# Kernel tuning notes

Hardware: AMD Instinct MI355X
Metric: run time of the kernel (lower is better)

The kernel has to match this reference:

```python
import jax, jax.numpy as jnp
import numpy as np


def setup_inputs() -> dict:
    key = jax.random.key(0)
    k1, k2, k3, k4 = jax.random.split(key, 4)
    B, L1, L2, H, A = 64, 512, 512, 1024, 1024
    reps_lt = jax.random.normal(k1, (B, L1, H), dtype=jnp.float32)
    reps_rt = jax.random.normal(k2, (B, L2, H), dtype=jnp.float32)
    mask_lt = jnp.ones((B, L1), dtype=jnp.float32)
    mask_rt = jnp.ones((B, L2), dtype=jnp.float32)
    # Keras 'uniform' initializer ~ U(-0.05, 0.05); scale similarly
    attn_w1 = jax.random.uniform(k3, (H, A), dtype=jnp.float32, minval=-0.05, maxval=0.05)
    diagonal_W = jax.random.uniform(k4, (1, 1, A), dtype=jnp.float32, minval=-0.05, maxval=0.05)
    return {
        "reps_lt": reps_lt,
        "reps_rt": reps_rt,
        "mask_lt": mask_lt,
        "mask_rt": mask_rt,
        "attn_w1": attn_w1,
        "diagonal_W": diagonal_W,
    }


def reference(reps_lt, reps_rt, mask_lt, mask_rt, attn_w1, diagonal_W):
    # Projections: the original does expand_dims + broadcast multiply + sum,
    # which is mathematically a matmul over the hidden dim.
    # attn_w2 aliases attn_w1 because hidden dims are equal.
    attn_lt = jnp.tanh(jnp.einsum('blh,ha->bla', reps_lt, attn_w1))  # [B,L1,A]
    attn_rt = jnp.tanh(jnp.einsum('brh,ha->bra', reps_rt, attn_w1))  # [B,L2,A]
    attn_lt = attn_lt * diagonal_W                                   # diagonal bilinear scale
    # batch_dot([B,L1,A], [B,A,L2]) -> [B,L1,L2]
    attn_value = jnp.einsum('bla,bra->blr', attn_lt, attn_rt)
    # mask (multiplicative, as in original) before softmax
    attn_value = attn_value * mask_lt[:, :, None] * mask_rt[:, None, :]
    attn_prob = jax.nn.softmax(attn_value, axis=-1)
    # mask again after softmax
    attn_prob = attn_prob * mask_lt[:, :, None] * mask_rt[:, None, :]
    return attn_prob
```

## Files before the change

kernel.cpp:

```cpp
#include <hip/hip_runtime.h>
#include <hip/hip_bf16.h>

#define B_ 64
#define L_ 512
#define H_ 1024
#define A_ 1024

typedef short bf16x8 __attribute__((ext_vector_type(8)));
typedef float f32x4 __attribute__((ext_vector_type(4)));

__device__ __forceinline__ void gld16(const void* g, void* l) {
  __builtin_amdgcn_global_load_lds((const __attribute__((address_space(1))) void*)g,
                                   (__attribute__((address_space(3))) void*)l, 16, 0, 0);
}

__device__ __forceinline__ unsigned short f2bf(float f) {
  unsigned u = __builtin_bit_cast(unsigned, f);
  u = (u + 0x7fffu + ((u >> 16) & 1u)) >> 16;
  return (unsigned short)u;
}

__device__ __forceinline__ unsigned short cvtbf(float f) {
  __hip_bfloat16 b = __float2bfloat16(f);
  return __builtin_bit_cast(unsigned short, b);
}

__device__ __forceinline__ float fast_tanh(float x) {
  float e = __expf(2.f * x);
  float r = __builtin_amdgcn_rcpf(e + 1.f);
  return __builtin_fmaf(-2.f, r, 1.f);
}

__global__ __launch_bounds__(256) void cvt_kernel(const float* __restrict__ lt,
                                                  const float* __restrict__ rt,
                                                  unsigned short* __restrict__ xb) {
  const size_t NC = (size_t)B_ * L_ * H_ / 8;
  size_t stride = (size_t)gridDim.x * blockDim.x;
  for (size_t c = (size_t)blockIdx.x * blockDim.x + threadIdx.x; c < 2 * NC; c += stride) {
    const float* src = (c < NC) ? (lt + c * 8) : (rt + (c - NC) * 8);
    float4 v0 = ((const float4*)src)[0];
    float4 v1 = ((const float4*)src)[1];
    bf16x8 o;
    o[0] = (short)cvtbf(v0.x); o[1] = (short)cvtbf(v0.y);
    o[2] = (short)cvtbf(v0.z); o[3] = (short)cvtbf(v0.w);
    o[4] = (short)cvtbf(v1.x); o[5] = (short)cvtbf(v1.y);
    o[6] = (short)cvtbf(v1.z); o[7] = (short)cvtbf(v1.w);
    *(bf16x8*)(xb + c * 8) = o;
  }
}

__global__ __launch_bounds__(256) void wtrans_kernel(const float* __restrict__ W,
                                                     unsigned short* __restrict__ Wt) {
  __shared__ float tile[32][33];
  int tx = threadIdx.x & 31, ty = threadIdx.x >> 5;
  int a0 = (blockIdx.x & 31) << 5, h0 = (blockIdx.x >> 5) << 5;
#pragma unroll
  for (int i = 0; i < 4; ++i) {
    int h = ty + i * 8;
    tile[h][tx] = W[(size_t)(h0 + h) * A_ + a0 + tx];
  }
  __syncthreads();
#pragma unroll
  for (int i = 0; i < 4; ++i) {
    int a = ty + i * 8;
    Wt[(size_t)(a0 + a) * H_ + h0 + tx] = f2bf(tile[tx][a]);
  }
}

#define STG_A(buf, h, kt) {                                                 \
    gld16(gA##h    + (kt) * 64, &As[buf][(h) * 8192 + lofs]);               \
    gld16(gA##h##b + (kt) * 64, &As[buf][(h) * 8192 + 4096 + lofs]); }
#define STG_B(buf, h, kt) {                                                 \
    gld16(gB##h    + (kt) * 64, &Bs[buf][(h) * 8192 + lofs]);               \
    gld16(gB##h##b + (kt) * 64, &Bs[buf][(h) * 8192 + 4096 + lofs]); }

#define LOAD_BQ(buf) { _Pragma("unroll") for (int ni = 0; ni < 4; ++ni) {   \
    int brow = wc * 64 + ni * 16 + l15;                                     \
    bq[ni][0] = *(const bf16x8*)&Bs[buf][brow * 64 + rd0];                  \
    bq[ni][1] = *(const bf16x8*)&Bs[buf][brow * 64 + rd1]; } }

#define PHASE(q, buf, STAGE_OP, CKPT) {                                     \
    bf16x8 aq0, aq1, aq2, aq3;                                              \
    { int ar = wr * 128 + (q) * 32 + l15;                                   \
      aq0 = *(const bf16x8*)&As[buf][ar * 64 + rd0];                        \
      aq1 = *(const bf16x8*)&As[buf][ar * 64 + rd1];                        \
      aq2 = *(const bf16x8*)&As[buf][(ar + 16) * 64 + rd0];                 \
      aq3 = *(const bf16x8*)&As[buf][(ar + 16) * 64 + rd1]; }               \
    STAGE_OP;                                                               \
    asm volatile("s_barrier" ::: "memory");                                 \
    __builtin_amdgcn_s_setprio(1);                                          \
    _Pragma("unroll") for (int ni = 0; ni < 4; ++ni) {                      \
      acc[(q)*2][ni] = __builtin_amdgcn_mfma_f32_16x16x32_bf16(             \
          aq0, bq[ni][0], acc[(q)*2][ni], 0, 0, 0);                         \
      acc[(q)*2][ni] = __builtin_amdgcn_mfma_f32_16x16x32_bf16(             \
          aq1, bq[ni][1], acc[(q)*2][ni], 0, 0, 0);                         \
      acc[(q)*2+1][ni] = __builtin_amdgcn_mfma_f32_16x16x32_bf16(           \
          aq2, bq[ni][0], acc[(q)*2+1][ni], 0, 0, 0);                       \
      acc[(q)*2+1][ni] = __builtin_amdgcn_mfma_f32_16x16x32_bf16(           \
          aq3, bq[ni][1], acc[(q)*2+1][ni], 0, 0, 0); }                     \
    __builtin_amdgcn_s_setprio(0);                                          \
    if (CKPT) asm volatile("s_waitcnt vmcnt(4)" ::: "memory");              \
    asm volatile("s_barrier" ::: "memory"); }

#define CONV_ITER(kt1, kt2, kt3) {                                          \
    LOAD_BQ(0);                                                             \
    PHASE(0, 0, STG_A(1, 0, kt1), 0);                                       \
    PHASE(1, 0, STG_A(1, 1, kt1), 0);                                       \
    PHASE(2, 0, STG_B(0, 0, kt2), 0);                                       \
    PHASE(3, 0, STG_B(0, 1, kt2), 1);                                       \
    LOAD_BQ(1);                                                             \
    PHASE(0, 1, STG_A(0, 0, kt2), 0);                                       \
    PHASE(1, 1, STG_A(0, 1, kt2), 0);                                       \
    PHASE(2, 1, STG_B(1, 0, kt3), 0);                                       \
    PHASE(3, 1, STG_B(1, 1, kt3), 1); }

#define CONVEYOR_LIT()                                                      \
  STG_B(0, 0, 0); STG_B(0, 1, 0);                                           \
  STG_A(0, 0, 0); STG_A(0, 1, 0);                                           \
  STG_B(1, 0, 1); STG_B(1, 1, 1);                                           \
  asm volatile("s_waitcnt vmcnt(4)" ::: "memory");                          \
  asm volatile("s_barrier" ::: "memory");                                   \
  CONV_ITER(1, 2, 3)   CONV_ITER(3, 4, 5)   CONV_ITER(5, 6, 7)              \
  CONV_ITER(7, 8, 9)   CONV_ITER(9, 10, 11) CONV_ITER(11, 12, 13)           \
  CONV_ITER(13, 14, 15) CONV_ITER(15, 0, 1)

__global__ __launch_bounds__(512, 2) void proj8_kernel(
    const unsigned short* __restrict__ Xb, const unsigned short* __restrict__ Wt,
    const float* __restrict__ diag, unsigned short* __restrict__ Pb) {
  __shared__ unsigned short As[2][256 * 64];
  __shared__ unsigned short Bs[2][256 * 64];
  int t = threadIdx.x;
  int lane = t & 63, wave = t >> 6;
  int wr = wave >> 2, wc = wave & 3;
  int l15 = lane & 15, l4 = lane >> 4;

  int bid = (int)blockIdx.x;
  int x = bid & 7, k = bid >> 3;
  int mt = x + 8 * (k >> 2);
  int nt = k & 3;
  int mrow0 = mt << 8, ncol0 = nt << 8;
  int isLt = (mt < 128);

  int rs = t >> 3, ss = t & 7;
  const unsigned short* gA0 = Xb + (size_t)(mrow0 + rs) * H_ + ((ss ^ (rs & 7)) << 3);
  const unsigned short* gA0b = gA0 + (size_t)64 * H_;
  const unsigned short* gA1  = gA0 + (size_t)128 * H_;
  const unsigned short* gA1b = gA0 + (size_t)192 * H_;
  const unsigned short* gB0 = Wt + (size_t)(ncol0 + rs) * H_ + ((ss ^ (rs & 7)) << 3);
  const unsigned short* gB0b = gB0 + (size_t)64 * H_;
  const unsigned short* gB1  = gB0 + (size_t)128 * H_;
  const unsigned short* gB1b = gB0 + (size_t)192 * H_;
  int lofs = (rs * 8 + ss) * 8;

  int rd0 = (l4 ^ (l15 & 7)) * 8;
  int rd1 = ((4 + l4) ^ (l15 & 7)) * 8;

  f32x4 acc[8][4] = {};
  bf16x8 bq[4][2];

  CONVEYOR_LIT();

#pragma unroll
  for (int mi = 0; mi < 8; ++mi) {
#pragma unroll
    for (int ni = 0; ni < 4; ++ni) {
      int col = ncol0 + wc * 64 + ni * 16 + l15;
      float d = isLt ? diag[col] : 1.0f;
#pragma unroll
      for (int rr = 0; rr < 4; ++rr) {
        int row = mrow0 + wr * 128 + mi * 16 + l4 * 4 + rr;
        Pb[(size_t)row * A_ + col] = f2bf(fast_tanh(acc[mi][ni][rr]) * d);
      }
    }
  }
}

__global__ __launch_bounds__(512) void ssmax_kernel(
    const unsigned short* __restrict__ Pb,
    const float* __restrict__ mask_lt, const float* __restrict__ mask_rt,
    float* __restrict__ out) {
  __shared__ unsigned short As2[3][128 * 32];
  __shared__ unsigned short Bs2[3][512 * 32];
  int t = threadIdx.x;
  int lane = t & 63, wave = t >> 6;
  int wr = wave >> 2, wc = wave & 3;
  int l15 = lane & 15, l4 = lane >> 4;

  int bid = (int)blockIdx.x;
  int g = (bid & 7) * 32 + (bid >> 3);
  int b = g >> 2, mt = g & 3;

  int arow0 = b * L_ + mt * 128;
  int brow0 = B_ * L_ + b * L_;

  int ra = t >> 2, ca = t & 3;
  const unsigned short* gA = Pb + (size_t)(arow0 + ra) * H_ + ((ca ^ ((ra >> 1) & 3)) << 3);
  const unsigned short* gBu0; const unsigned short* gBu1;
  const unsigned short* gBu2; const unsigned short* gBu3;
  int bd0, bd1, bd2, bd3;
  {
    int ci, r, c;
    ci = t;           r = ci >> 2; c = ci & 3;
    gBu0 = Pb + (size_t)(brow0 + r) * H_ + ((c ^ ((r >> 1) & 3)) << 3); bd0 = ci * 8;
    ci = 512 + t;     r = ci >> 2; c = ci & 3;
    gBu1 = Pb + (size_t)(brow0 + r) * H_ + ((c ^ ((r >> 1) & 3)) << 3); bd1 = ci * 8;
    ci = 1024 + t;    r = ci >> 2; c = ci & 3;
    gBu2 = Pb + (size_t)(brow0 + r) * H_ + ((c ^ ((r >> 1) & 3)) << 3); bd2 = ci * 8;
    ci = 1536 + t;    r = ci >> 2; c = ci & 3;
    gBu3 = Pb + (size_t)(brow0 + r) * H_ + ((c ^ ((r >> 1) & 3)) << 3); bd3 = ci * 8;
  }
  int rd = (l4 ^ ((l15 >> 1) & 3)) * 8;

#define SSTG_B01(buf, kt_) { int ko = (kt_) * 32;                  \
    gld16(gBu0 + ko, &Bs2[buf][bd0]); gld16(gBu1 + ko, &Bs2[buf][bd1]); }
#define SSTG_B23A(buf, kt_) { int ko = (kt_) * 32;                 \
    gld16(gBu2 + ko, &Bs2[buf][bd2]); gld16(gBu3 + ko, &Bs2[buf][bd3]); \
    gld16(gA + ko, &As2[buf][t * 8]); }

  f32x4 acc[4][8] = {};

  SSTG_B01(0, 0); SSTG_B23A(0, 0);
  SSTG_B01(1, 1); SSTG_B23A(1, 1);
  asm volatile("s_waitcnt vmcnt(5)" ::: "memory");
  asm volatile("s_barrier" ::: "memory");

#pragma unroll 1
  for (int j = 0; j < 32; ++j) {
    int buf = j - (j / 3) * 3;
    int nb = buf + 2; if (nb >= 3) nb -= 3;
    bool st = (j <= 29);
    const unsigned short* Ac = As2[buf];
    const unsigned short* Bc = Bs2[buf];

    bf16x8 aq[4], bq[4];
#pragma unroll
    for (int mi = 0; mi < 4; ++mi)
      aq[mi] = *(const bf16x8*)&Ac[(wr * 64 + mi * 16 + l15) * 32 + rd];
#pragma unroll
    for (int ni = 0; ni < 4; ++ni)
      bq[ni] = *(const bf16x8*)&Bc[(wc * 128 + ni * 16 + l15) * 32 + rd];
    if (st) SSTG_B01(nb, j + 2);
    asm volatile("s_barrier" ::: "memory");
    __builtin_amdgcn_s_setprio(1);
#pragma unroll
    for (int mi = 0; mi < 4; ++mi)
#pragma unroll
      for (int ni = 0; ni < 4; ++ni)
        acc[mi][ni] = __builtin_amdgcn_mfma_f32_16x16x32_bf16(aq[mi], bq[ni], acc[mi][ni], 0, 0, 0);
    __builtin_amdgcn_s_setprio(0);
    asm volatile("s_barrier" ::: "memory");

#pragma unroll
    for (int ni = 0; ni < 4; ++ni)
      bq[ni] = *(const bf16x8*)&Bc[(wc * 128 + 64 + ni * 16 + l15) * 32 + rd];
    if (st) SSTG_B23A(nb, j + 2);
    asm volatile("s_barrier" ::: "memory");
    __builtin_amdgcn_s_setprio(1);
#pragma unroll
    for (int mi = 0; mi < 4; ++mi)
#pragma unroll
      for (int ni = 0; ni < 4; ++ni)
        acc[mi][ni + 4] = __builtin_amdgcn_mfma_f32_16x16x32_bf16(aq[mi], bq[ni], acc[mi][ni + 4], 0, 0, 0);
    __builtin_amdgcn_s_setprio(0);
    if (j < 30)
      asm volatile("s_waitcnt vmcnt(5)" ::: "memory");
    else
      asm volatile("s_waitcnt vmcnt(0)" ::: "memory");
    asm volatile("s_barrier" ::: "memory");
  }
#undef SSTG_B01
#undef SSTG_B23A

  float* red = (float*)&As2[0][0];
  float* red2 = red + 512;

  float ml[4][4];
#pragma unroll
  for (int mi = 0; mi < 4; ++mi)
#pragma unroll
    for (int rr = 0; rr < 4; ++rr)
      ml[mi][rr] = mask_lt[b * L_ + mt * 128 + wr * 64 + mi * 16 + l4 * 4 + rr];
  float mr[8];
#pragma unroll
  for (int ni = 0; ni < 8; ++ni)
    mr[ni] = mask_rt[b * L_ + wc * 128 + ni * 16 + l15];

#pragma unroll
  for (int mi = 0; mi < 4; ++mi)
#pragma unroll
    for (int ni = 0; ni < 8; ++ni)
#pragma unroll
      for (int rr = 0; rr < 4; ++rr)
        acc[mi][ni][rr] *= ml[mi][rr] * mr[ni];

#pragma unroll
  for (int mi = 0; mi < 4; ++mi)
#pragma unroll
    for (int rr = 0; rr < 4; ++rr) {
      float m = acc[mi][0][rr];
#pragma unroll
      for (int ni = 1; ni < 8; ++ni) m = fmaxf(m, acc[mi][ni][rr]);
      m = fmaxf(m, __shfl_xor(m, 1));
      m = fmaxf(m, __shfl_xor(m, 2));
      m = fmaxf(m, __shfl_xor(m, 4));
      m = fmaxf(m, __shfl_xor(m, 8));
      if (l15 == 0) red[(wr * 64 + mi * 16 + l4 * 4 + rr) * 4 + wc] = m;
    }
  __syncthreads();
  float mfull[4][4];
#pragma unroll
  for (int mi = 0; mi < 4; ++mi)
#pragma unroll
    for (int rr = 0; rr < 4; ++rr) {
      float4 v = *(const float4*)&red[(wr * 64 + mi * 16 + l4 * 4 + rr) * 4];
      mfull[mi][rr] = fmaxf(fmaxf(v.x, v.y), fmaxf(v.z, v.w));
    }

#pragma unroll
  for (int mi = 0; mi < 4; ++mi)
#pragma unroll
    for (int rr = 0; rr < 4; ++rr) {
      float s = 0.f;
#pragma unroll
      for (int ni = 0; ni < 8; ++ni) {
        float e = __expf(acc[mi][ni][rr] - mfull[mi][rr]);
        acc[mi][ni][rr] = e;
        s += e;
      }
      s += __shfl_xor(s, 1);
      s += __shfl_xor(s, 2);
      s += __shfl_xor(s, 4);
      s += __shfl_xor(s, 8);
      if (l15 == 0) red2[(wr * 64 + mi * 16 + l4 * 4 + rr) * 4 + wc] = s;
    }
  __syncthreads();

  float* obase = out + (size_t)b * L_ * L_ + (size_t)(mt * 128) * L_;
#pragma unroll
  for (int mi = 0; mi < 4; ++mi)
#pragma unroll
    for (int rr = 0; rr < 4; ++rr) {
      int row = wr * 64 + mi * 16 + l4 * 4 + rr;
      float4 v = *(const float4*)&red2[row * 4];
      float inv = 1.0f / (((v.x + v.y) + (v.z + v.w)));
      float scale = inv * ml[mi][rr];
#pragma unroll
      for (int ni = 0; ni < 8; ++ni) {
        int col = wc * 128 + ni * 16 + l15;
        obase[(size_t)row * L_ + col] = acc[mi][ni][rr] * scale * mr[ni];
      }
    }
}

extern "C" void kernel_launch(void* const* d_in, const int* in_sizes, int n_in,
                              void* d_out, int out_size, void* d_ws, size_t ws_size,
                              hipStream_t stream) {
  const float* reps_lt = (const float*)d_in[0];
  const float* reps_rt = (const float*)d_in[1];
  const float* mask_lt = (const float*)d_in[2];
  const float* mask_rt = (const float*)d_in[3];
  const float* attn_w1 = (const float*)d_in[4];
  const float* diag    = (const float*)d_in[5];
  float* out = (float*)d_out;

  unsigned short* wt = (unsigned short*)d_ws;
  unsigned short* pb = wt + (size_t)H_ * A_;
  unsigned short* xb = pb + (size_t)B_ * L_ * A_ * 2;

  hipLaunchKernelGGL(wtrans_kernel, dim3(1024), dim3(256), 0, stream, attn_w1, wt);
  hipLaunchKernelGGL(cvt_kernel, dim3(8192), dim3(256), 0, stream,
                     reps_lt, reps_rt, xb);
  hipLaunchKernelGGL(proj8_kernel, dim3(1024), dim3(512), 0, stream,
                     xb, wt, diag, pb);
  hipLaunchKernelGGL(ssmax_kernel, dim3(256), dim3(512), 0, stream,
                     pb, mask_lt, mask_rt, out);
}
```

Measured before the change: 281.4 us.

## Fuse fp32-to-bf16 input conversion into projection GEMM A-operand staging

Removes the separate conversion kernel that read the fp32 activations and wrote a bf16 copy to workspace. The projection GEMM now loads fp32 A tiles into registers, converts them to bf16 and writes them into LDS inside the software pipeline, while B tiles keep using direct global-to-LDS loads. This saves a full pass over the input plus the bf16 write and re-read. In exchange, each A tile is now fetched as fp32 by every N-tile block, which doubles A-operand global traffic. The kernel also holds 32 extra VGPRs of staging registers at two blocks per CU, which risks spills or occupancy pressure.

```diff
diff --git a/kernel.cpp b/kernel.cpp
--- a/kernel.cpp
+++ b/kernel.cpp
@@ -29,24 +29,6 @@
   float e = __expf(2.f * x);
   float r = __builtin_amdgcn_rcpf(e + 1.f);
   return __builtin_fmaf(-2.f, r, 1.f);
-}
-
-__global__ __launch_bounds__(256) void cvt_kernel(const float* __restrict__ lt,
-                                                  const float* __restrict__ rt,
-                                                  unsigned short* __restrict__ xb) {
-  const size_t NC = (size_t)B_ * L_ * H_ / 8;
-  size_t stride = (size_t)gridDim.x * blockDim.x;
-  for (size_t c = (size_t)blockIdx.x * blockDim.x + threadIdx.x; c < 2 * NC; c += stride) {
-    const float* src = (c < NC) ? (lt + c * 8) : (rt + (c - NC) * 8);
-    float4 v0 = ((const float4*)src)[0];
-    float4 v1 = ((const float4*)src)[1];
-    bf16x8 o;
-    o[0] = (short)cvtbf(v0.x); o[1] = (short)cvtbf(v0.y);
-    o[2] = (short)cvtbf(v0.z); o[3] = (short)cvtbf(v0.w);
-    o[4] = (short)cvtbf(v1.x); o[5] = (short)cvtbf(v1.y);
-    o[6] = (short)cvtbf(v1.z); o[7] = (short)cvtbf(v1.w);
-    *(bf16x8*)(xb + c * 8) = o;
-  }
 }
 
 __global__ __launch_bounds__(256) void wtrans_kernel(const float* __restrict__ W,
@@ -67,26 +49,43 @@
   }
 }
 
-#define STG_A(buf, h, kt) {                                                 \
-    gld16(gA##h    + (kt) * 64, &As[buf][(h) * 8192 + lofs]);               \
-    gld16(gA##h##b + (kt) * 64, &As[buf][(h) * 8192 + 4096 + lofs]); }
 #define STG_B(buf, h, kt) {                                                 \
     gld16(gB##h    + (kt) * 64, &Bs[buf][(h) * 8192 + lofs]);               \
     gld16(gB##h##b + (kt) * 64, &Bs[buf][(h) * 8192 + 4096 + lofs]); }
+
+#define AISSUE(SET, kt) {                                                   \
+    const float* p0 = gAf##SET  + (kt) * 64;                                \
+    const float* p1 = gAf##SET##b + (kt) * 64;                              \
+    rA##SET##_0 = ((const float4*)p0)[0]; rA##SET##_1 = ((const float4*)p0)[1]; \
+    rA##SET##_2 = ((const float4*)p1)[0]; rA##SET##_3 = ((const float4*)p1)[1]; }
+
+#define AWRITE(SET, buf) {                                                  \
+    bf16x8 v0, v1;                                                          \
+    v0[0] = (short)cvtbf(rA##SET##_0.x); v0[1] = (short)cvtbf(rA##SET##_0.y); \
+    v0[2] = (short)cvtbf(rA##SET##_0.z); v0[3] = (short)cvtbf(rA##SET##_0.w); \
+    v0[4] = (short)cvtbf(rA##SET##_1.x); v0[5] = (short)cvtbf(rA##SET##_1.y); \
+    v0[6] = (short)cvtbf(rA##SET##_1.z); v0[7] = (short)cvtbf(rA##SET##_1.w); \
+    v1[0] = (short)cvtbf(rA##SET##_2.x); v1[1] = (short)cvtbf(rA##SET##_2.y); \
+    v1[2] = (short)cvtbf(rA##SET##_2.z); v1[3] = (short)cvtbf(rA##SET##_2.w); \
+    v1[4] = (short)cvtbf(rA##SET##_3.x); v1[5] = (short)cvtbf(rA##SET##_3.y); \
+    v1[6] = (short)cvtbf(rA##SET##_3.z); v1[7] = (short)cvtbf(rA##SET##_3.w); \
+    *(bf16x8*)&As[buf][(SET) * 8192 + lofs] = v0;                           \
+    *(bf16x8*)&As[buf][(SET) * 8192 + 4096 + lofs] = v1;                    \
+    asm volatile("s_waitcnt lgkmcnt(0)" ::: "memory"); }
 
 #define LOAD_BQ(buf) { _Pragma("unroll") for (int ni = 0; ni < 4; ++ni) {   \
     int brow = wc * 64 + ni * 16 + l15;                                     \
     bq[ni][0] = *(const bf16x8*)&Bs[buf][brow * 64 + rd0];                  \
     bq[ni][1] = *(const bf16x8*)&Bs[buf][brow * 64 + rd1]; } }
 
-#define PHASE(q, buf, STAGE_OP, CKPT) {                                     \
+#define PHASE(q, buf, PRE_OP, POST_OP, CKPT) {                              \
     bf16x8 aq0, aq1, aq2, aq3;                                              \
     { int ar = wr * 128 + (q) * 32 + l15;                                   \
       aq0 = *(const bf16x8*)&As[buf][ar * 64 + rd0];                        \
       aq1 = *(const bf16x8*)&As[buf][ar * 64 + rd1];                        \
       aq2 = *(const bf16x8*)&As[buf][(ar + 16) * 64 + rd0];                 \
       aq3 = *(const bf16x8*)&As[buf][(ar + 16) * 64 + rd1]; }               \
-    STAGE_OP;                                                               \
+    PRE_OP;                                                                 \
     asm volatile("s_barrier" ::: "memory");                                 \
     __builtin_amdgcn_s_setprio(1);                                          \
     _Pragma("unroll") for (int ni = 0; ni < 4; ++ni) {                      \
@@ -99,34 +98,26 @@
       acc[(q)*2+1][ni] = __builtin_amdgcn_mfma_f32_16x16x32_bf16(           \
           aq3, bq[ni][1], acc[(q)*2+1][ni], 0, 0, 0); }                     \
     __builtin_amdgcn_s_setprio(0);                                          \
+    POST_OP;                                                                \
     if (CKPT) asm volatile("s_waitcnt vmcnt(4)" ::: "memory");              \
     asm volatile("s_barrier" ::: "memory"); }
 
-#define CONV_ITER(kt1, kt2, kt3) {                                          \
+#define CONV_ITER_F(kt1, kt2, kt3) {                                        \
     LOAD_BQ(0);                                                             \
-    PHASE(0, 0, STG_A(1, 0, kt1), 0);                                       \
-    PHASE(1, 0, STG_A(1, 1, kt1), 0);                                       \
-    PHASE(2, 0, STG_B(0, 0, kt2), 0);                                       \
-    PHASE(3, 0, STG_B(0, 1, kt2), 1);                                       \
+    PHASE(0, 0, AISSUE(0, kt1), ;, 0);                                      \
+    PHASE(1, 0, AISSUE(1, kt1), ;, 0);                                      \
+    PHASE(2, 0, STG_B(0, 0, kt2), AWRITE(0, 1), 0);                         \
+    PHASE(3, 0, STG_B(0, 1, kt2), AWRITE(1, 1), 1);                         \
     LOAD_BQ(1);                                                             \
-    PHASE(0, 1, STG_A(0, 0, kt2), 0);                                       \
-    PHASE(1, 1, STG_A(0, 1, kt2), 0);                                       \
-    PHASE(2, 1, STG_B(1, 0, kt3), 0);                                       \
-    PHASE(3, 1, STG_B(1, 1, kt3), 1); }
-
-#define CONVEYOR_LIT()                                                      \
-  STG_B(0, 0, 0); STG_B(0, 1, 0);                                           \
-  STG_A(0, 0, 0); STG_A(0, 1, 0);                                           \
-  STG_B(1, 0, 1); STG_B(1, 1, 1);                                           \
-  asm volatile("s_waitcnt vmcnt(4)" ::: "memory");                          \
-  asm volatile("s_barrier" ::: "memory");                                   \
-  CONV_ITER(1, 2, 3)   CONV_ITER(3, 4, 5)   CONV_ITER(5, 6, 7)              \
-  CONV_ITER(7, 8, 9)   CONV_ITER(9, 10, 11) CONV_ITER(11, 12, 13)           \
-  CONV_ITER(13, 14, 15) CONV_ITER(15, 0, 1)
+    PHASE(0, 1, AISSUE(0, kt2), ;, 0);                                      \
+    PHASE(1, 1, AISSUE(1, kt2), ;, 0);                                      \
+    PHASE(2, 1, STG_B(1, 0, kt3), AWRITE(0, 0), 0);                         \
+    PHASE(3, 1, STG_B(1, 1, kt3), AWRITE(1, 0), 1); }
 
 __global__ __launch_bounds__(512, 2) void proj8_kernel(
-    const unsigned short* __restrict__ Xb, const unsigned short* __restrict__ Wt,
-    const float* __restrict__ diag, unsigned short* __restrict__ Pb) {
+    const float* __restrict__ Xlt, const float* __restrict__ Xrt,
+    const unsigned short* __restrict__ Wt, const float* __restrict__ diag,
+    unsigned short* __restrict__ Pb) {
   __shared__ unsigned short As[2][256 * 64];
   __shared__ unsigned short Bs[2][256 * 64];
   int t = threadIdx.x;
@@ -140,12 +131,14 @@
   int nt = k & 3;
   int mrow0 = mt << 8, ncol0 = nt << 8;
   int isLt = (mt < 128);
+  const float* X = isLt ? Xlt : Xrt;
+  int xrow0 = (isLt ? mt : mt - 128) << 8;
 
   int rs = t >> 3, ss = t & 7;
-  const unsigned short* gA0 = Xb + (size_t)(mrow0 + rs) * H_ + ((ss ^ (rs & 7)) << 3);
-  const unsigned short* gA0b = gA0 + (size_t)64 * H_;
-  const unsigned short* gA1  = gA0 + (size_t)128 * H_;
-  const unsigned short* gA1b = gA0 + (size_t)192 * H_;
+  const float* gAf0  = X + (size_t)(xrow0 + rs) * H_ + ((ss ^ (rs & 7)) * 8);
+  const float* gAf0b = gAf0 + (size_t)64 * H_;
+  const float* gAf1  = gAf0 + (size_t)128 * H_;
+  const float* gAf1b = gAf0 + (size_t)192 * H_;
   const unsigned short* gB0 = Wt + (size_t)(ncol0 + rs) * H_ + ((ss ^ (rs & 7)) << 3);
   const unsigned short* gB0b = gB0 + (size_t)64 * H_;
   const unsigned short* gB1  = gB0 + (size_t)128 * H_;
@@ -157,8 +150,19 @@
 
   f32x4 acc[8][4] = {};
   bf16x8 bq[4][2];
-
-  CONVEYOR_LIT();
+  float4 rA0_0, rA0_1, rA0_2, rA0_3;
+  float4 rA1_0, rA1_1, rA1_2, rA1_3;
+
+  AISSUE(0, 0); AISSUE(1, 0);
+  STG_B(0, 0, 0); STG_B(0, 1, 0);
+  AWRITE(0, 0); AWRITE(1, 0);
+  STG_B(1, 0, 1); STG_B(1, 1, 1);
+  asm volatile("s_waitcnt vmcnt(4)" ::: "memory");
+  asm volatile("s_barrier" ::: "memory");
+
+  CONV_ITER_F(1, 2, 3)    CONV_ITER_F(3, 4, 5)    CONV_ITER_F(5, 6, 7)
+  CONV_ITER_F(7, 8, 9)    CONV_ITER_F(9, 10, 11)  CONV_ITER_F(11, 12, 13)
+  CONV_ITER_F(13, 14, 15) CONV_ITER_F(15, 0, 1)
 
 #pragma unroll
   for (int mi = 0; mi < 8; ++mi) {
@@ -200,13 +204,13 @@
   int bd0, bd1, bd2, bd3;
   {
     int ci, r, c;
-    ci = t;           r = ci >> 2; c = ci & 3;
+    ci = t;        r = ci >> 2; c = ci & 3;
     gBu0 = Pb + (size_t)(brow0 + r) * H_ + ((c ^ ((r >> 1) & 3)) << 3); bd0 = ci * 8;
-    ci = 512 + t;     r = ci >> 2; c = ci & 3;
+    ci = 512 + t;  r = ci >> 2; c = ci & 3;
     gBu1 = Pb + (size_t)(brow0 + r) * H_ + ((c ^ ((r >> 1) & 3)) << 3); bd1 = ci * 8;
-    ci = 1024 + t;    r = ci >> 2; c = ci & 3;
+    ci = 1024 + t; r = ci >> 2; c = ci & 3;
     gBu2 = Pb + (size_t)(brow0 + r) * H_ + ((c ^ ((r >> 1) & 3)) << 3); bd2 = ci * 8;
-    ci = 1536 + t;    r = ci >> 2; c = ci & 3;
+    ci = 1536 + t; r = ci >> 2; c = ci & 3;
     gBu3 = Pb + (size_t)(brow0 + r) * H_ + ((c ^ ((r >> 1) & 3)) << 3); bd3 = ci * 8;
   }
   int rd = (l4 ^ ((l15 >> 1) & 3)) * 8;
@@ -365,13 +369,10 @@
 
   unsigned short* wt = (unsigned short*)d_ws;
   unsigned short* pb = wt + (size_t)H_ * A_;
-  unsigned short* xb = pb + (size_t)B_ * L_ * A_ * 2;
 
   hipLaunchKernelGGL(wtrans_kernel, dim3(1024), dim3(256), 0, stream, attn_w1, wt);
-  hipLaunchKernelGGL(cvt_kernel, dim3(8192), dim3(256), 0, stream,
-                     reps_lt, reps_rt, xb);
   hipLaunchKernelGGL(proj8_kernel, dim3(1024), dim3(512), 0, stream,
-                     xb, wt, diag, pb);
+                     reps_lt, reps_rt, wt, diag, pb);
   hipLaunchKernelGGL(ssmax_kernel, dim3(256), dim3(512), 0, stream,
                      pb, mask_lt, mask_rt, out);
 }
```

New measurement: 302.9 us. +7.6%, slower.
